# Performance work log

Hardware: AMD Instinct MI355X
Metric: run time of the kernel (lower is better)

## Reference

```python
import jax, jax.numpy as jnp
import numpy as np

TAU = 2.0      # membrane time constant
V_TH = 1.0     # spike threshold (v_reset = 0, hard reset)
T_STEPS = 4    # num_steps

@jax.custom_vjp
def heaviside_atan(x):
    # forward: Heaviside; backward: spikingjelly ATan surrogate (alpha=2)
    return (x >= 0.0).astype(x.dtype)

def _h_fwd(x):
    return heaviside_atan(x), x

def _h_bwd(x, g):
    alpha = 2.0
    return (g * (alpha / 2.0) / (1.0 + (jnp.pi / 2.0 * alpha * x) ** 2),)

heaviside_atan.defvjp(_h_fwd, _h_bwd)

def lif_multistep(x_seq):
    # spikingjelly LIFNode, step_mode='m', decay_input=True, v_reset=0, detach_reset=True
    def step(v, x):
        v = v + (x - v) / TAU                      # charge
        s = heaviside_atan(v - V_TH)               # fire (surrogate grad)
        v = v * (1.0 - jax.lax.stop_gradient(s))   # hard reset, detached spike
        return v, s
    v0 = jnp.zeros_like(x_seq[0])
    _, spikes = jax.lax.scan(step, v0, x_seq)
    return spikes

def setup_inputs() -> dict:
    key = jax.random.key(0)
    k0, k1, k2 = jax.random.split(key, 3)
    B, L, C, D, NL = 16, 512, 128, 1024, 2
    inputs = jax.random.normal(k0, (B, L, C), jnp.float32)
    enc_W = jax.random.normal(k1, (C, D), jnp.float32) / np.sqrt(C).astype(np.float32)
    enc_b = jnp.zeros((D,), jnp.float32)
    W_cells = jax.random.normal(k2, (NL, D, D), jnp.float32) / np.sqrt(D).astype(np.float32)
    b_cells = jnp.zeros((NL, D), jnp.float32)
    return {"inputs": inputs, "enc_W": enc_W, "enc_b": enc_b,
            "W_cells": W_cells, "b_cells": b_cells}

def reference(inputs, enc_W, enc_b, W_cells, b_cells):
    # temporal spike encoder: repeat input over T steps, LIF-encode to spikes
    x = jnp.swapaxes(inputs, 1, 2)                       # [B, C, L]
    x = jnp.broadcast_to(x[None], (T_STEPS,) + x.shape)  # [T, B, C, L]
    h = lif_multistep(x)
    h = jnp.swapaxes(h, -2, -1)                          # [T, B, L, C]
    # encoder linear + init LIF
    h = lif_multistep(h @ enc_W + enc_b)                 # [T, B, L, D]
    # stacked SpikeRNNCells: Linear(D,D) -> multistep LIF
    for i in range(W_cells.shape[0]):
        h = lif_multistep(h @ W_cells[i] + b_cells[i])
    out = h.mean(0)                                      # [B, L, D]
    return out, out.mean(axis=1)                         # ([B,L,D], [B,D])
```

## Files before the change

kernel.cpp:

```cpp
#include <hip/hip_runtime.h>
#include <hip/hip_bf16.h>
#include <stdint.h>

#define TSTEPS 4

typedef __bf16 bf16_t;
typedef __attribute__((ext_vector_type(8))) __bf16 bf16x8;
typedef __attribute__((ext_vector_type(16))) float f32x16;
typedef __attribute__((ext_vector_type(4))) unsigned short ushort4v;

union frag_u { bf16x8 v; uint32_t d[4]; unsigned short u[8]; };

#define VMCNT12 0xF7C
#define VMCNT6  0xF76
#define VMCNT0  0xF70


__global__ void spike_encode_i8(const float* __restrict__ x,
                                uint4* __restrict__ s1)
{
    const int C = 128;
    int tid = blockIdx.x * blockDim.x + threadIdx.x;
    int row = tid & 31;
    int kb  = (tid >> 5) & 7;
    int m_blk = tid >> 8;
    int m = m_blk * 32 + row;
    const float* px = x + (size_t)m * C + kb * 16;
    float xv[16];
#pragma unroll
    for (int j = 0; j < 16; j += 4) {
        float4 t4 = *(const float4*)(px + j);
        xv[j] = t4.x; xv[j+1] = t4.y; xv[j+2] = t4.z; xv[j+3] = t4.w;
    }
    float v[16];
#pragma unroll
    for (int j = 0; j < 16; ++j) v[j] = 0.0f;
#pragma unroll
    for (int t = 0; t < TSTEPS; ++t) {
        uint32_t dw[4] = {0u, 0u, 0u, 0u};
#pragma unroll
        for (int j = 0; j < 16; ++j) {
            float vv = __fadd_rn(v[j], __fmul_rn(__fsub_rn(xv[j], v[j]), 0.5f));
            bool sp = (vv >= 1.0f);
            dw[j >> 2] |= sp ? (0x3Fu << ((j & 3) * 8)) : 0u;
            v[j] = sp ? 0.0f : vv;
        }
        uint4 o; o.x = dw[0]; o.y = dw[1]; o.z = dw[2]; o.w = dw[3];
        s1[((size_t)(m_blk * 8 + kb) * 4 + t) * 32 + row] = o;
    }
}

__global__ void split_transpose_all(const float* __restrict__ enc_W,
                                    const float* __restrict__ W_cells,
                                    bf16_t* __restrict__ W1h, bf16_t* __restrict__ W1l,
                                    bf16_t* __restrict__ W2h, bf16_t* __restrict__ W2l,
                                    bf16_t* __restrict__ W3h, bf16_t* __restrict__ W3l)
{
    const int N = 1024;
    const float* W;
    bf16_t *hi, *lo;
    int K;
    if (blockIdx.z == 0) {
        if (blockIdx.x >= 4) return;
        W = enc_W; hi = W1h; lo = W1l; K = 128;
    } else if (blockIdx.z == 1) {
        W = W_cells; hi = W2h; lo = W2l; K = 1024;
    } else {
        W = W_cells + (size_t)1024 * 1024; hi = W3h; lo = W3l; K = 1024;
    }
    const int NKB = K >> 4;
    __shared__ float tile[32][33];
    int k0 = blockIdx.x * 32, n0 = blockIdx.y * 32;
    int tx = threadIdx.x & 31, ty = threadIdx.x >> 5;
    for (int kk = ty; kk < 32; kk += 8)
        tile[kk][tx] = W[(size_t)(k0 + kk) * N + n0 + tx];
    __syncthreads();

    const int nn = tx;
    const int oc = ty;
    const int o2 = oc & 3;
    const bool isLo = (oc >> 2) != 0;
    const int kblk = (k0 >> 4) + (o2 >> 1);
    const int lane_in_packet = nn + 32 * (o2 & 1);

    frag_u f;
#pragma unroll
    for (int j = 0; j < 8; ++j) {
        float wv = tile[o2 * 8 + j][nn];
        bf16_t h = (bf16_t)wv;
        bf16_t l = (bf16_t)(wv - (float)h);
        f.v[j] = isLo ? (bf16_t)(2.0f * (float)l)
                      : (bf16_t)(2.0f * (float)h);
    }
    bf16_t* dst = (isLo ? lo : hi)
        + ((size_t)((n0 + nn) >> 5) * NKB + kblk) * 512 + lane_in_packet * 8;
    *(bf16x8*)dst = f.v;
}

template <int K, bool LAST>
__global__ __launch_bounds__(256, 4)
void gemm_lif_mfma(const uint8_t* __restrict__ Abytes,
                   const bf16_t* __restrict__ Bh,
                   const bf16_t* __restrict__ Bl,
                   const float* __restrict__ bias,
                   uint8_t* __restrict__ Sbytes,
                   float* __restrict__ Out,
                   int M, int N)
{
    constexpr int NKB = K >> 4;
    __shared__ __align__(8) unsigned short sh[4][256];

    const int tid = threadIdx.x;
    const int lane = tid & 63;
    const int wid = tid >> 6;
    const int l31 = lane & 31;
    const int half = lane >> 5;

    const int bid = blockIdx.x;
    const int xcd = bid & 7;
    const int j   = bid >> 3;
    const int nh   = j >> 7;
    const int r    = j & 127;
    const int mloc = r >> 3;
    const int n_t  = nh * 8 + (r & 7);
    const int m_t  = xcd * 16 + mloc;

    const int m0 = m_t * 64, n0 = n_t * 64;
    const int wave_m = (wid & 1) * 32;
    const int wave_n = (wid >> 1) * 32;
    const int m_blk = (m0 + wave_m) >> 5;
    const int n_blk = (n0 + wave_n) >> 5;

    const uint8_t* pA = Abytes + (size_t)m_blk * NKB * 4 * 512 + l31 * 16 + half * 8;
    const bf16_t* pH = Bh + (size_t)n_blk * NKB * 512 + lane * 8;
    const bf16_t* pL = Bl + (size_t)n_blk * NKB * 512 + lane * 8;

    f32x16 acc[TSTEPS];
#pragma unroll
    for (int t = 0; t < TSTEPS; ++t)
        for (int rr = 0; rr < 16; ++rr) acc[t][rr] = 0.0f;

    uint2 fm[4][4];
    bf16x8 fh[4], fl[4];

#define LOADB(kb_, s_) {                                                     \
        fm[s_][0] = *(const uint2*)(pA + ((size_t)(kb_) * 4 + 0) * 512);     \
        fm[s_][1] = *(const uint2*)(pA + ((size_t)(kb_) * 4 + 1) * 512);     \
        fm[s_][2] = *(const uint2*)(pA + ((size_t)(kb_) * 4 + 2) * 512);     \
        fm[s_][3] = *(const uint2*)(pA + ((size_t)(kb_) * 4 + 3) * 512);     \
        fh[s_] = *(const bf16x8*)(pH + (kb_) * 512);                         \
        fl[s_] = *(const bf16x8*)(pL + (kb_) * 512);                         \
    }

#define EXPANDF(a_, f_) {                                                    \
        (f_).d[0] = __builtin_amdgcn_perm((a_).x, 0u, 0x05000400u);          \
        (f_).d[1] = __builtin_amdgcn_perm((a_).x, 0u, 0x07000600u);          \
        (f_).d[2] = __builtin_amdgcn_perm((a_).y, 0u, 0x05000400u);          \
        (f_).d[3] = __builtin_amdgcn_perm((a_).y, 0u, 0x07000600u);          \
    }

#define MFMASTEP(s_) {                                                       \
        frag_u af0, af1, af2, af3;                                           \
        EXPANDF(fm[s_][0], af0);                                             \
        EXPANDF(fm[s_][1], af1);                                             \
        EXPANDF(fm[s_][2], af2);                                             \
        EXPANDF(fm[s_][3], af3);                                             \
        acc[0] = __builtin_amdgcn_mfma_f32_32x32x16_bf16(af0.v, fh[s_], acc[0], 0, 0, 0); \
        acc[1] = __builtin_amdgcn_mfma_f32_32x32x16_bf16(af1.v, fh[s_], acc[1], 0, 0, 0); \
        acc[2] = __builtin_amdgcn_mfma_f32_32x32x16_bf16(af2.v, fh[s_], acc[2], 0, 0, 0); \
        acc[3] = __builtin_amdgcn_mfma_f32_32x32x16_bf16(af3.v, fh[s_], acc[3], 0, 0, 0); \
        acc[0] = __builtin_amdgcn_mfma_f32_32x32x16_bf16(af0.v, fl[s_], acc[0], 0, 0, 0); \
        acc[1] = __builtin_amdgcn_mfma_f32_32x32x16_bf16(af1.v, fl[s_], acc[1], 0, 0, 0); \
        acc[2] = __builtin_amdgcn_mfma_f32_32x32x16_bf16(af2.v, fl[s_], acc[2], 0, 0, 0); \
        acc[3] = __builtin_amdgcn_mfma_f32_32x32x16_bf16(af3.v, fl[s_], acc[3], 0, 0, 0); \
    }

#define STEPP(kb_, s_) {                                                     \
        LOADB((kb_) + 2, ((s_) + 2) & 3);                                    \
        __builtin_amdgcn_s_waitcnt(VMCNT12);                                 \
        asm volatile("" ::: "memory");                                       \
        MFMASTEP(s_);                                                        \
    }
#define STEPW(s_, w_) {                                                      \
        __builtin_amdgcn_s_waitcnt(w_);                                      \
        asm volatile("" ::: "memory");                                       \
        MFMASTEP(s_);                                                        \
    }

    LOADB(0, 0);
    LOADB(1, 1);
    for (int kb = 0; kb < NKB - 4; kb += 4) {
        STEPP(kb + 0, 0);
        STEPP(kb + 1, 1);
        STEPP(kb + 2, 2);
        STEPP(kb + 3, 3);
    }
    STEPP(NKB - 4, 0);
    STEPP(NKB - 3, 1);
    STEPW(2, VMCNT6);
    STEPW(3, VMCNT0);

#undef STEPW
#undef STEPP
#undef MFMASTEP
#undef EXPANDF
#undef LOADB

    const float bv = bias[n0 + wave_n + l31];
    f32x16 vmem;
#pragma unroll
    for (int rr = 0; rr < 16; ++rr) vmem[rr] = 0.0f;
    uint64_t bits = 0ull;
    unsigned short* myt = &sh[wid][0];

    const int NKBo = N >> 4;
    const int kbase = (n0 + wave_n) >> 4;

    for (int t = 0; t < TSTEPS; ++t) {
#pragma unroll
        for (int rr = 0; rr < 16; ++rr) {
            float y = __fadd_rn(acc[t][rr], bv);
            float vv = vmem[rr];
            vv = __fadd_rn(vv, __fmul_rn(__fsub_rn(y, vv), 0.5f));
            bool sp = (vv >= 1.0f);
            vmem[rr] = sp ? 0.0f : vv;
            if (LAST) {
                bits |= sp ? (1ull << (rr * 4 + t)) : 0ull;
            } else {
                unsigned long long b = __ballot(sp);
                if (l31 == 0) {
                    uint32_t hb = (uint32_t)(b >> (half * 32));
                    int rowi = (rr & 3) + 8 * (rr >> 2) + 4 * half;
                    myt[(rowi * 2 + 0) * 4 + t] = (unsigned short)hb;
                    myt[(rowi * 2 + 1) * 4 + t] = (unsigned short)(hb >> 16);
                }
            }
        }
    }

    if (LAST) {
#pragma unroll
        for (int rr = 0; rr < 16; ++rr) {
            int m_r = (rr & 3) + 8 * (rr >> 2) + 4 * half;
            int m = m0 + wave_m + m_r;
            int n = n0 + wave_n + l31;
            int cnt = __popc((unsigned)((bits >> (rr * 4)) & 0xFull));
            Out[(size_t)m * N + n] = 0.25f * (float)cnt;
        }
    } else {
        const ushort4v pk = *(const ushort4v*)&myt[(l31 * 2 + half) * 4];
#pragma unroll
        for (int t = 0; t < TSTEPS; ++t) {
            uint32_t m16 = pk[t];
            uint4 o;
            o.x = (((m16      ) & 0xFu) * 0x00204081u & 0x01010101u) * 0x3Fu;
            o.y = (((m16 >>  4) & 0xFu) * 0x00204081u & 0x01010101u) * 0x3Fu;
            o.z = (((m16 >>  8) & 0xFu) * 0x00204081u & 0x01010101u) * 0x3Fu;
            o.w = (((m16 >> 12) & 0xFu) * 0x00204081u & 0x01010101u) * 0x3Fu;
            *(uint4*)(Sbytes + ((((size_t)m_blk * NKBo + kbase + half) * 4 + t)
                                * 32 + l31) * 16) = o;
        }
    }
}

__global__ void zero_out2(float* __restrict__ out2, int n)
{
    int i = blockIdx.x * blockDim.x + threadIdx.x;
    if (i < n) out2[i] = 0.0f;
}

__global__ void mean_over_L_atomic(const float* __restrict__ out,
                                   float* __restrict__ out2,
                                   int B, int L, int D)
{
    int id = blockIdx.x * blockDim.x + threadIdx.x;
    int bd = id & (B * D - 1);
    int chunk = id >> 14;
    int b = bd >> 10, d = bd & (D - 1);
    const float* p = out + (size_t)b * L * D + (size_t)chunk * 64 * D + d;
    float s = 0.0f;
#pragma unroll 8
    for (int l = 0; l < 64; ++l) s += p[(size_t)l * D];
    atomicAdd(out2 + bd, s * (1.0f / 512.0f));
}

extern "C" void kernel_launch(void* const* d_in, const int* in_sizes, int n_in,
                              void* d_out, int out_size, void* d_ws, size_t ws_size,
                              hipStream_t stream)
{
    const float* inputs  = (const float*)d_in[0];
    const float* enc_W   = (const float*)d_in[1];
    const float* enc_b   = (const float*)d_in[2];
    const float* W_cells = (const float*)d_in[3];
    const float* b_cells = (const float*)d_in[4];

    const int B = 16, L = 512, C = 128, D = 1024;
    const int M = B * L;

    char* ws = (char*)d_ws;
    size_t off = 0;
    uint8_t* s1 = (uint8_t*)(ws + off);
    off += (size_t)(M / 32) * (C / 16) * 4 * 32 * 16;
    bf16_t* W1h = (bf16_t*)(ws + off); off += (size_t)C * D * 2;
    bf16_t* W1l = (bf16_t*)(ws + off); off += (size_t)C * D * 2;
    bf16_t* W2h = (bf16_t*)(ws + off); off += (size_t)D * D * 2;
    bf16_t* W2l = (bf16_t*)(ws + off); off += (size_t)D * D * 2;
    bf16_t* W3h = (bf16_t*)(ws + off); off += (size_t)D * D * 2;
    bf16_t* W3l = (bf16_t*)(ws + off); off += (size_t)D * D * 2;
    uint8_t* h0 = (uint8_t*)(ws + off);
    off += (size_t)(M / 32) * (D / 16) * 4 * 32 * 16;
    uint8_t* h1 = (uint8_t*)(ws + off);

    float* out  = (float*)d_out;
    float* out2 = out + (size_t)M * D;

    split_transpose_all<<<dim3(32, 32, 3), 256, 0, stream>>>(
        enc_W, W_cells, W1h, W1l, W2h, W2l, W3h, W3l);

    spike_encode_i8<<<256, 256, 0, stream>>>(inputs, (uint4*)s1);

    zero_out2<<<(B * D + 255) / 256, 256, 0, stream>>>(out2, B * D);

    const int nblocks = (M / 64) * (D / 64);
    gemm_lif_mfma<128, false><<<nblocks, 256, 0, stream>>>(
        s1, W1h, W1l, enc_b, h0, nullptr, M, D);
    gemm_lif_mfma<1024, false><<<nblocks, 256, 0, stream>>>(
        h0, W2h, W2l, b_cells, h1, nullptr, M, D);
    gemm_lif_mfma<1024, true><<<nblocks, 256, 0, stream>>>(
        h1, W3h, W3l, b_cells + D, nullptr, out, M, D);

    mean_over_L_atomic<<<(B * D * 8) / 256, 256, 0, stream>>>(
        out, out2, B, L, D);
}
```

Baseline: 326.5 us.

## Widen per-wave GEMM tile to 32x64 to reuse spike A fragments

Each wave now computes two 32-column N subtiles, so the block tile grows from 64x64 to 64x128 and the grid shrinks by half. The A spike fragments, and the byte-to-bf16 expansion done on them, are loaded and expanded once and reused for both B subtiles, cutting A traffic and permute ALU work per output. The register prefetch pipeline goes from four stages to two (one k-block ahead), and launch bounds drop to 2 blocks per CU to fit the doubled accumulators. The shallower prefetch and lower occupancy risk exposing more memory latency.

Result: no change. 332.8 us (+1.9%).

```diff
diff --git a/kernel.cpp b/kernel.cpp
--- a/kernel.cpp
+++ b/kernel.cpp
@@ -11,8 +11,7 @@
 
 union frag_u { bf16x8 v; uint32_t d[4]; unsigned short u[8]; };
 
-#define VMCNT12 0xF7C
-#define VMCNT6  0xF76
+#define VMCNT8  0xF78
 #define VMCNT0  0xF70
 
 
@@ -98,7 +97,7 @@
 }
 
 template <int K, bool LAST>
-__global__ __launch_bounds__(256, 4)
+__global__ __launch_bounds__(256, 2)
 void gemm_lif_mfma(const uint8_t* __restrict__ Abytes,
                    const bf16_t* __restrict__ Bh,
                    const bf16_t* __restrict__ Bl,
@@ -119,37 +118,41 @@
     const int bid = blockIdx.x;
     const int xcd = bid & 7;
     const int j   = bid >> 3;
-    const int nh   = j >> 7;
-    const int r    = j & 127;
-    const int mloc = r >> 3;
-    const int n_t  = nh * 8 + (r & 7);
+    const int nh   = j >> 6;
+    const int r    = j & 63;
+    const int mloc = r >> 2;
+    const int n_t  = nh * 4 + (r & 3);
     const int m_t  = xcd * 16 + mloc;
 
-    const int m0 = m_t * 64, n0 = n_t * 64;
+    const int m0 = m_t * 64, n0 = n_t * 128;
     const int wave_m = (wid & 1) * 32;
-    const int wave_n = (wid >> 1) * 32;
+    const int wave_n = (wid >> 1) * 64;
     const int m_blk = (m0 + wave_m) >> 5;
     const int n_blk = (n0 + wave_n) >> 5;
 
     const uint8_t* pA = Abytes + (size_t)m_blk * NKB * 4 * 512 + l31 * 16 + half * 8;
-    const bf16_t* pH = Bh + (size_t)n_blk * NKB * 512 + lane * 8;
-    const bf16_t* pL = Bl + (size_t)n_blk * NKB * 512 + lane * 8;
-
-    f32x16 acc[TSTEPS];
+    const bf16_t* pH0 = Bh + (size_t)n_blk * NKB * 512 + lane * 8;
+    const bf16_t* pL0 = Bl + (size_t)n_blk * NKB * 512 + lane * 8;
+    const bf16_t* pH1 = pH0 + (size_t)NKB * 512;
+    const bf16_t* pL1 = pL0 + (size_t)NKB * 512;
+
+    f32x16 acc0[TSTEPS], acc1[TSTEPS];
 #pragma unroll
     for (int t = 0; t < TSTEPS; ++t)
-        for (int rr = 0; rr < 16; ++rr) acc[t][rr] = 0.0f;
-
-    uint2 fm[4][4];
-    bf16x8 fh[4], fl[4];
+        for (int rr = 0; rr < 16; ++rr) { acc0[t][rr] = 0.0f; acc1[t][rr] = 0.0f; }
+
+    uint2 fm[2][4];
+    bf16x8 fh0[2], fl0[2], fh1[2], fl1[2];
 
 #define LOADB(kb_, s_) {                                                     \
         fm[s_][0] = *(const uint2*)(pA + ((size_t)(kb_) * 4 + 0) * 512);     \
         fm[s_][1] = *(const uint2*)(pA + ((size_t)(kb_) * 4 + 1) * 512);     \
         fm[s_][2] = *(const uint2*)(pA + ((size_t)(kb_) * 4 + 2) * 512);     \
         fm[s_][3] = *(const uint2*)(pA + ((size_t)(kb_) * 4 + 3) * 512);     \
-        fh[s_] = *(const bf16x8*)(pH + (kb_) * 512);                         \
-        fl[s_] = *(const bf16x8*)(pL + (kb_) * 512);                         \
+        fh0[s_] = *(const bf16x8*)(pH0 + (kb_) * 512);                       \
+        fl0[s_] = *(const bf16x8*)(pL0 + (kb_) * 512);                       \
+        fh1[s_] = *(const bf16x8*)(pH1 + (kb_) * 512);                       \
+        fl1[s_] = *(const bf16x8*)(pL1 + (kb_) * 512);                       \
     }
 
 #define EXPANDF(a_, f_) {                                                    \
@@ -165,102 +168,107 @@
         EXPANDF(fm[s_][1], af1);                                             \
         EXPANDF(fm[s_][2], af2);                                             \
         EXPANDF(fm[s_][3], af3);                                             \
-        acc[0] = __builtin_amdgcn_mfma_f32_32x32x16_bf16(af0.v, fh[s_], acc[0], 0, 0, 0); \
-        acc[1] = __builtin_amdgcn_mfma_f32_32x32x16_bf16(af1.v, fh[s_], acc[1], 0, 0, 0); \
-        acc[2] = __builtin_amdgcn_mfma_f32_32x32x16_bf16(af2.v, fh[s_], acc[2], 0, 0, 0); \
-        acc[3] = __builtin_amdgcn_mfma_f32_32x32x16_bf16(af3.v, fh[s_], acc[3], 0, 0, 0); \
-        acc[0] = __builtin_amdgcn_mfma_f32_32x32x16_bf16(af0.v, fl[s_], acc[0], 0, 0, 0); \
-        acc[1] = __builtin_amdgcn_mfma_f32_32x32x16_bf16(af1.v, fl[s_], acc[1], 0, 0, 0); \
-        acc[2] = __builtin_amdgcn_mfma_f32_32x32x16_bf16(af2.v, fl[s_], acc[2], 0, 0, 0); \
-        acc[3] = __builtin_amdgcn_mfma_f32_32x32x16_bf16(af3.v, fl[s_], acc[3], 0, 0, 0); \
-    }
-
-#define STEPP(kb_, s_) {                                                     \
-        LOADB((kb_) + 2, ((s_) + 2) & 3);                                    \
-        __builtin_amdgcn_s_waitcnt(VMCNT12);                                 \
-        asm volatile("" ::: "memory");                                       \
-        MFMASTEP(s_);                                                        \
-    }
-#define STEPW(s_, w_) {                                                      \
-        __builtin_amdgcn_s_waitcnt(w_);                                      \
-        asm volatile("" ::: "memory");                                       \
-        MFMASTEP(s_);                                                        \
+        acc0[0] = __builtin_amdgcn_mfma_f32_32x32x16_bf16(af0.v, fh0[s_], acc0[0], 0, 0, 0); \
+        acc1[0] = __builtin_amdgcn_mfma_f32_32x32x16_bf16(af0.v, fh1[s_], acc1[0], 0, 0, 0); \
+        acc0[1] = __builtin_amdgcn_mfma_f32_32x32x16_bf16(af1.v, fh0[s_], acc0[1], 0, 0, 0); \
+        acc1[1] = __builtin_amdgcn_mfma_f32_32x32x16_bf16(af1.v, fh1[s_], acc1[1], 0, 0, 0); \
+        acc0[2] = __builtin_amdgcn_mfma_f32_32x32x16_bf16(af2.v, fh0[s_], acc0[2], 0, 0, 0); \
+        acc1[2] = __builtin_amdgcn_mfma_f32_32x32x16_bf16(af2.v, fh1[s_], acc1[2], 0, 0, 0); \
+        acc0[3] = __builtin_amdgcn_mfma_f32_32x32x16_bf16(af3.v, fh0[s_], acc0[3], 0, 0, 0); \
+        acc1[3] = __builtin_amdgcn_mfma_f32_32x32x16_bf16(af3.v, fh1[s_], acc1[3], 0, 0, 0); \
+        acc0[0] = __builtin_amdgcn_mfma_f32_32x32x16_bf16(af0.v, fl0[s_], acc0[0], 0, 0, 0); \
+        acc1[0] = __builtin_amdgcn_mfma_f32_32x32x16_bf16(af0.v, fl1[s_], acc1[0], 0, 0, 0); \
+        acc0[1] = __builtin_amdgcn_mfma_f32_32x32x16_bf16(af1.v, fl0[s_], acc0[1], 0, 0, 0); \
+        acc1[1] = __builtin_amdgcn_mfma_f32_32x32x16_bf16(af1.v, fl1[s_], acc1[1], 0, 0, 0); \
+        acc0[2] = __builtin_amdgcn_mfma_f32_32x32x16_bf16(af2.v, fl0[s_], acc0[2], 0, 0, 0); \
+        acc1[2] = __builtin_amdgcn_mfma_f32_32x32x16_bf16(af2.v, fl1[s_], acc1[2], 0, 0, 0); \
+        acc0[3] = __builtin_amdgcn_mfma_f32_32x32x16_bf16(af3.v, fl0[s_], acc0[3], 0, 0, 0); \
+        acc1[3] = __builtin_amdgcn_mfma_f32_32x32x16_bf16(af3.v, fl1[s_], acc1[3], 0, 0, 0); \
     }
 
     LOADB(0, 0);
-    LOADB(1, 1);
-    for (int kb = 0; kb < NKB - 4; kb += 4) {
-        STEPP(kb + 0, 0);
-        STEPP(kb + 1, 1);
-        STEPP(kb + 2, 2);
-        STEPP(kb + 3, 3);
-    }
-    STEPP(NKB - 4, 0);
-    STEPP(NKB - 3, 1);
-    STEPW(2, VMCNT6);
-    STEPW(3, VMCNT0);
-
-#undef STEPW
-#undef STEPP
+    for (int kb = 0; kb < NKB - 2; kb += 2) {
+        LOADB(kb + 1, 1);
+        __builtin_amdgcn_s_waitcnt(VMCNT8);
+        asm volatile("" ::: "memory");
+        MFMASTEP(0);
+        LOADB(kb + 2, 0);
+        __builtin_amdgcn_s_waitcnt(VMCNT8);
+        asm volatile("" ::: "memory");
+        MFMASTEP(1);
+    }
+    LOADB(NKB - 1, 1);
+    __builtin_amdgcn_s_waitcnt(VMCNT8);
+    asm volatile("" ::: "memory");
+    MFMASTEP(0);
+    __builtin_amdgcn_s_waitcnt(VMCNT0);
+    asm volatile("" ::: "memory");
+    MFMASTEP(1);
+
 #undef MFMASTEP
 #undef EXPANDF
 #undef LOADB
 
-    const float bv = bias[n0 + wave_n + l31];
-    f32x16 vmem;
-#pragma unroll
-    for (int rr = 0; rr < 16; ++rr) vmem[rr] = 0.0f;
-    uint64_t bits = 0ull;
     unsigned short* myt = &sh[wid][0];
-
     const int NKBo = N >> 4;
-    const int kbase = (n0 + wave_n) >> 4;
-
-    for (int t = 0; t < TSTEPS; ++t) {
-#pragma unroll
-        for (int rr = 0; rr < 16; ++rr) {
-            float y = __fadd_rn(acc[t][rr], bv);
-            float vv = vmem[rr];
-            vv = __fadd_rn(vv, __fmul_rn(__fsub_rn(y, vv), 0.5f));
-            bool sp = (vv >= 1.0f);
-            vmem[rr] = sp ? 0.0f : vv;
-            if (LAST) {
-                bits |= sp ? (1ull << (rr * 4 + t)) : 0ull;
-            } else {
-                unsigned long long b = __ballot(sp);
-                if (l31 == 0) {
-                    uint32_t hb = (uint32_t)(b >> (half * 32));
-                    int rowi = (rr & 3) + 8 * (rr >> 2) + 4 * half;
-                    myt[(rowi * 2 + 0) * 4 + t] = (unsigned short)hb;
-                    myt[(rowi * 2 + 1) * 4 + t] = (unsigned short)(hb >> 16);
-                }
-            }
-        }
-    }
-
-    if (LAST) {
-#pragma unroll
-        for (int rr = 0; rr < 16; ++rr) {
-            int m_r = (rr & 3) + 8 * (rr >> 2) + 4 * half;
-            int m = m0 + wave_m + m_r;
-            int n = n0 + wave_n + l31;
-            int cnt = __popc((unsigned)((bits >> (rr * 4)) & 0xFull));
-            Out[(size_t)m * N + n] = 0.25f * (float)cnt;
-        }
-    } else {
-        const ushort4v pk = *(const ushort4v*)&myt[(l31 * 2 + half) * 4];
-#pragma unroll
-        for (int t = 0; t < TSTEPS; ++t) {
-            uint32_t m16 = pk[t];
-            uint4 o;
-            o.x = (((m16      ) & 0xFu) * 0x00204081u & 0x01010101u) * 0x3Fu;
-            o.y = (((m16 >>  4) & 0xFu) * 0x00204081u & 0x01010101u) * 0x3Fu;
-            o.z = (((m16 >>  8) & 0xFu) * 0x00204081u & 0x01010101u) * 0x3Fu;
-            o.w = (((m16 >> 12) & 0xFu) * 0x00204081u & 0x01010101u) * 0x3Fu;
-            *(uint4*)(Sbytes + ((((size_t)m_blk * NKBo + kbase + half) * 4 + t)
-                                * 32 + l31) * 16) = o;
-        }
-    }
+
+#define EPILOG(acc_, nidx_) {                                                \
+        const float bv = bias[n0 + wave_n + (nidx_) * 32 + l31];             \
+        f32x16 vmem;                                                         \
+        _Pragma("unroll")                                                    \
+        for (int rr = 0; rr < 16; ++rr) vmem[rr] = 0.0f;                     \
+        uint64_t bits = 0ull;                                                \
+        for (int t = 0; t < TSTEPS; ++t) {                                   \
+            _Pragma("unroll")                                                \
+            for (int rr = 0; rr < 16; ++rr) {                                \
+                float y = __fadd_rn(acc_[t][rr], bv);                        \
+                float vv = vmem[rr];                                         \
+                vv = __fadd_rn(vv, __fmul_rn(__fsub_rn(y, vv), 0.5f));       \
+                bool sp = (vv >= 1.0f);                                      \
+                vmem[rr] = sp ? 0.0f : vv;                                   \
+                if (LAST) {                                                  \
+                    bits |= sp ? (1ull << (rr * 4 + t)) : 0ull;              \
+                } else {                                                     \
+                    unsigned long long b = __ballot(sp);                     \
+                    if (l31 == 0) {                                          \
+                        uint32_t hb = (uint32_t)(b >> (half * 32));          \
+                        int rowi = (rr & 3) + 8 * (rr >> 2) + 4 * half;      \
+                        myt[(rowi * 2 + 0) * 4 + t] = (unsigned short)hb;    \
+                        myt[(rowi * 2 + 1) * 4 + t] = (unsigned short)(hb >> 16); \
+                    }                                                        \
+                }                                                            \
+            }                                                                \
+        }                                                                    \
+        if (LAST) {                                                          \
+            _Pragma("unroll")                                                \
+            for (int rr = 0; rr < 16; ++rr) {                                \
+                int m_r = (rr & 3) + 8 * (rr >> 2) + 4 * half;               \
+                int m = m0 + wave_m + m_r;                                   \
+                int n = n0 + wave_n + (nidx_) * 32 + l31;                    \
+                int cnt = __popc((unsigned)((bits >> (rr * 4)) & 0xFull));   \
+                Out[(size_t)m * N + n] = 0.25f * (float)cnt;                 \
+            }                                                                \
+        } else {                                                             \
+            const int kbase = (n0 + wave_n + (nidx_) * 32) >> 4;             \
+            const ushort4v pk = *(const ushort4v*)&myt[(l31 * 2 + half) * 4];\
+            _Pragma("unroll")                                                \
+            for (int t = 0; t < TSTEPS; ++t) {                               \
+                uint32_t m16 = pk[t];                                        \
+                uint4 o;                                                     \
+                o.x = (((m16      ) & 0xFu) * 0x00204081u & 0x01010101u) * 0x3Fu; \
+                o.y = (((m16 >>  4) & 0xFu) * 0x00204081u & 0x01010101u) * 0x3Fu; \
+                o.z = (((m16 >>  8) & 0xFu) * 0x00204081u & 0x01010101u) * 0x3Fu; \
+                o.w = (((m16 >> 12) & 0xFu) * 0x00204081u & 0x01010101u) * 0x3Fu; \
+                *(uint4*)(Sbytes + ((((size_t)m_blk * NKBo + kbase + half) * 4 + t) \
+                                    * 32 + l31) * 16) = o;                   \
+            }                                                                \
+        }                                                                    \
+    }
+
+    EPILOG(acc0, 0);
+    EPILOG(acc1, 1);
+
+#undef EPILOG
 }
 
 __global__ void zero_out2(float* __restrict__ out2, int n)
@@ -321,7 +329,7 @@
 
     zero_out2<<<(B * D + 255) / 256, 256, 0, stream>>>(out2, B * D);
 
-    const int nblocks = (M / 64) * (D / 64);
+    const int nblocks = (M / 64) * (D / 128);
     gemm_lif_mfma<128, false><<<nblocks, 256, 0, stream>>>(
         s1, W1h, W1l, enc_b, h0, nullptr, M, D);
     gemm_lif_mfma<1024, false><<<nblocks, 256, 0, stream>>>(
```

## Stage B weight fragments through LDS with global_load_lds double buffering

Applied to the files above, without the earlier changes.

Previously every wave loaded its own B (hi/lo bf16) fragments straight from global memory, so waves sharing an N tile duplicated those loads. Now each wave issues one global_load_lds of a B slice into a double-buffered LDS tile, and waves read the fragments they need from LDS. The pipeline depth drops from a 4-stage register prefetch to a 2-stage double buffer, with a block barrier every k-step. This halves redundant global B traffic in exchange for extra LDS reads and barrier synchronisation.

Measured after the change: 317.1 us. -2.9%, faster.

```diff
diff --git a/kernel.cpp b/kernel.cpp
--- a/kernel.cpp
+++ b/kernel.cpp
@@ -11,9 +11,9 @@
 
 union frag_u { bf16x8 v; uint32_t d[4]; unsigned short u[8]; };
 
-#define VMCNT12 0xF7C
-#define VMCNT6  0xF76
-#define VMCNT0  0xF70
+#define WT_VM5_LG0  0x075
+#define WT_VM4      0xF74
+#define WT_VM0_LG0  0x070
 
 
 __global__ void spike_encode_i8(const float* __restrict__ x,
@@ -108,6 +108,7 @@
                    int M, int N)
 {
     constexpr int NKB = K >> 4;
+    __shared__ __align__(16) uint8_t ldsB[2][4096];
     __shared__ __align__(8) unsigned short sh[4][256];
 
     const int tid = threadIdx.x;
@@ -132,24 +133,30 @@
     const int n_blk = (n0 + wave_n) >> 5;
 
     const uint8_t* pA = Abytes + (size_t)m_blk * NKB * 4 * 512 + l31 * 16 + half * 8;
-    const bf16_t* pH = Bh + (size_t)n_blk * NKB * 512 + lane * 8;
-    const bf16_t* pL = Bl + (size_t)n_blk * NKB * 512 + lane * 8;
+
+    const uint8_t* stage_src = (const uint8_t*)(((wid & 1) ? Bl : Bh)
+        + (size_t)((n0 >> 5) + (wid >> 1)) * NKB * 512) + (lane << 4);
+    const uint8_t* ldsRd = &ldsB[0][0] + ((wid >> 1) << 11) + (lane << 4);
 
     f32x16 acc[TSTEPS];
 #pragma unroll
     for (int t = 0; t < TSTEPS; ++t)
         for (int rr = 0; rr < 16; ++rr) acc[t][rr] = 0.0f;
 
-    uint2 fm[4][4];
-    bf16x8 fh[4], fl[4];
-
-#define LOADB(kb_, s_) {                                                     \
+    uint2 fm[2][4];
+
+#define STAGE(kb_, b_)                                                        \
+    __builtin_amdgcn_global_load_lds(                                         \
+        (const __attribute__((address_space(1))) uint32_t*)                   \
+            (stage_src + (size_t)(kb_) * 1024),                               \
+        (__attribute__((address_space(3))) uint32_t*)(&ldsB[b_][wid << 10]),  \
+        16, 0, 0);
+
+#define LOADA(kb_, s_) {                                                     \
         fm[s_][0] = *(const uint2*)(pA + ((size_t)(kb_) * 4 + 0) * 512);     \
         fm[s_][1] = *(const uint2*)(pA + ((size_t)(kb_) * 4 + 1) * 512);     \
         fm[s_][2] = *(const uint2*)(pA + ((size_t)(kb_) * 4 + 2) * 512);     \
         fm[s_][3] = *(const uint2*)(pA + ((size_t)(kb_) * 4 + 3) * 512);     \
-        fh[s_] = *(const bf16x8*)(pH + (kb_) * 512);                         \
-        fl[s_] = *(const bf16x8*)(pL + (kb_) * 512);                         \
     }
 
 #define EXPANDF(a_, f_) {                                                    \
@@ -159,52 +166,61 @@
         (f_).d[3] = __builtin_amdgcn_perm((a_).y, 0u, 0x07000600u);          \
     }
 
-#define MFMASTEP(s_) {                                                       \
+#define MFMAS(s_, fhv_, flv_) {                                              \
         frag_u af0, af1, af2, af3;                                           \
         EXPANDF(fm[s_][0], af0);                                             \
         EXPANDF(fm[s_][1], af1);                                             \
         EXPANDF(fm[s_][2], af2);                                             \
         EXPANDF(fm[s_][3], af3);                                             \
-        acc[0] = __builtin_amdgcn_mfma_f32_32x32x16_bf16(af0.v, fh[s_], acc[0], 0, 0, 0); \
-        acc[1] = __builtin_amdgcn_mfma_f32_32x32x16_bf16(af1.v, fh[s_], acc[1], 0, 0, 0); \
-        acc[2] = __builtin_amdgcn_mfma_f32_32x32x16_bf16(af2.v, fh[s_], acc[2], 0, 0, 0); \
-        acc[3] = __builtin_amdgcn_mfma_f32_32x32x16_bf16(af3.v, fh[s_], acc[3], 0, 0, 0); \
-        acc[0] = __builtin_amdgcn_mfma_f32_32x32x16_bf16(af0.v, fl[s_], acc[0], 0, 0, 0); \
-        acc[1] = __builtin_amdgcn_mfma_f32_32x32x16_bf16(af1.v, fl[s_], acc[1], 0, 0, 0); \
-        acc[2] = __builtin_amdgcn_mfma_f32_32x32x16_bf16(af2.v, fl[s_], acc[2], 0, 0, 0); \
-        acc[3] = __builtin_amdgcn_mfma_f32_32x32x16_bf16(af3.v, fl[s_], acc[3], 0, 0, 0); \
-    }
-
-#define STEPP(kb_, s_) {                                                     \
-        LOADB((kb_) + 2, ((s_) + 2) & 3);                                    \
-        __builtin_amdgcn_s_waitcnt(VMCNT12);                                 \
+        acc[0] = __builtin_amdgcn_mfma_f32_32x32x16_bf16(af0.v, fhv_, acc[0], 0, 0, 0); \
+        acc[1] = __builtin_amdgcn_mfma_f32_32x32x16_bf16(af1.v, fhv_, acc[1], 0, 0, 0); \
+        acc[2] = __builtin_amdgcn_mfma_f32_32x32x16_bf16(af2.v, fhv_, acc[2], 0, 0, 0); \
+        acc[3] = __builtin_amdgcn_mfma_f32_32x32x16_bf16(af3.v, fhv_, acc[3], 0, 0, 0); \
+        acc[0] = __builtin_amdgcn_mfma_f32_32x32x16_bf16(af0.v, flv_, acc[0], 0, 0, 0); \
+        acc[1] = __builtin_amdgcn_mfma_f32_32x32x16_bf16(af1.v, flv_, acc[1], 0, 0, 0); \
+        acc[2] = __builtin_amdgcn_mfma_f32_32x32x16_bf16(af2.v, flv_, acc[2], 0, 0, 0); \
+        acc[3] = __builtin_amdgcn_mfma_f32_32x32x16_bf16(af3.v, flv_, acc[3], 0, 0, 0); \
+    }
+
+#define STEP(kb_, p_) {                                                      \
+        STAGE((kb_) + 1, (p_) ^ 1);                                          \
+        LOADA((kb_) + 1, (p_) ^ 1);                                          \
+        bf16x8 fhv = *(const bf16x8*)(ldsRd + (p_) * 4096);                  \
+        bf16x8 flv = *(const bf16x8*)(ldsRd + (p_) * 4096 + 1024);           \
+        __builtin_amdgcn_s_waitcnt(WT_VM5_LG0);                              \
         asm volatile("" ::: "memory");                                       \
-        MFMASTEP(s_);                                                        \
-    }
-#define STEPW(s_, w_) {                                                      \
-        __builtin_amdgcn_s_waitcnt(w_);                                      \
+        MFMAS(p_, fhv, flv);                                                 \
+        __builtin_amdgcn_s_waitcnt(WT_VM4);                                  \
         asm volatile("" ::: "memory");                                       \
-        MFMASTEP(s_);                                                        \
-    }
-
-    LOADB(0, 0);
-    LOADB(1, 1);
-    for (int kb = 0; kb < NKB - 4; kb += 4) {
-        STEPP(kb + 0, 0);
-        STEPP(kb + 1, 1);
-        STEPP(kb + 2, 2);
-        STEPP(kb + 3, 3);
-    }
-    STEPP(NKB - 4, 0);
-    STEPP(NKB - 3, 1);
-    STEPW(2, VMCNT6);
-    STEPW(3, VMCNT0);
-
-#undef STEPW
-#undef STEPP
-#undef MFMASTEP
+        __builtin_amdgcn_s_barrier();                                        \
+        asm volatile("" ::: "memory");                                       \
+    }
+
+    STAGE(0, 0);
+    LOADA(0, 0);
+    __builtin_amdgcn_s_waitcnt(WT_VM4);
+    asm volatile("" ::: "memory");
+    __builtin_amdgcn_s_barrier();
+    asm volatile("" ::: "memory");
+
+    for (int kb = 0; kb < NKB - 2; kb += 2) {
+        STEP(kb + 0, 0);
+        STEP(kb + 1, 1);
+    }
+    STEP(NKB - 2, 0);
+    {
+        bf16x8 fhv = *(const bf16x8*)(ldsRd + 4096);
+        bf16x8 flv = *(const bf16x8*)(ldsRd + 4096 + 1024);
+        __builtin_amdgcn_s_waitcnt(WT_VM0_LG0);
+        asm volatile("" ::: "memory");
+        MFMAS(1, fhv, flv);
+    }
+
+#undef STEP
+#undef MFMAS
 #undef EXPANDF
-#undef LOADB
+#undef LOADA
+#undef STAGE
 
     const float bv = bias[n0 + wave_n + l31];
     f32x16 vmem;
```
